# Kernel tuning notes

Hardware: AMD Instinct MI355X
Metric: run time of the kernel (lower is better)

The kernel has to match this reference:

```python
import jax, jax.numpy as jnp
import numpy as np

DELTA = 6.0      # 3 / (1 - alpha), alpha = 0.5
ETA = 1.0
MS_ITER = 3
D_FEAT = 256
N_PTS = 8192
X_SCALE = 0.06   # keeps ||x||^2 ~ 0.9 so exp(DELTA * X^T X) is well-conditioned


def setup_inputs() -> dict:
    key = jax.random.key(0)
    X = jax.random.normal(key, (D_FEAT, N_PTS), dtype=jnp.float32) * X_SCALE
    return {"X": X}


def _mean_shift_once(X):
    # X: [d, N]
    S = jnp.einsum('dn,dm->nm', X, X)          # X^T X, [N, N]
    K = jnp.exp(DELTA * S)                     # Gaussian-like affinity, [N, N]
    colsum = jnp.sum(K, axis=0)                # d = K^T @ ones  -> column sums, [N]
    # X @ P with P = (1-eta) I + eta K D_inv; D_inv = diag(1/colsum).
    # X @ K @ D_inv == (X @ K) / colsum (per-column scaling) -- no diag/eye materialized.
    XK = X @ K                                 # [d, N]
    return (1.0 - ETA) * X + ETA * (XK / colsum[None, :])


def reference(X):
    outs = []
    cur = X
    for _ in range(MS_ITER):
        cur = _mean_shift_once(cur)
        outs.append(cur)
    return tuple(outs)
```

## Files before the change

kernel.cpp:

```cpp
#include <hip/hip_runtime.h>
#include <hip/hip_bf16.h>
#include <stdint.h>

#define DFEAT 256
#define NPTS  8192

typedef __attribute__((ext_vector_type(8)))  short bf16x8;
typedef __attribute__((ext_vector_type(16))) float f32x16;
typedef __attribute__((ext_vector_type(4)))  int   int4v;
typedef __attribute__((ext_vector_type(4)))  float f32x4;

#define AS1 __attribute__((address_space(1)))
#define AS3 __attribute__((address_space(3)))

__device__ inline void dma16(const void* g, void* l) {
  __builtin_amdgcn_global_load_lds((const AS1 uint32_t*)g, (AS3 uint32_t*)l, 16, 0, 0);
}

__device__ inline uint16_t f2bf(float f) {
  union { float f; uint32_t u; } v; v.f = f;
  return (uint16_t)((v.u + 0x7FFFu + ((v.u >> 16) & 1u)) >> 16);
}

__device__ inline void barrier_lgkm_only() {
  __asm__ __volatile__("" ::: "memory");
  __builtin_amdgcn_s_waitcnt(0xC07F);
  __builtin_amdgcn_s_barrier();
  __asm__ __volatile__("" ::: "memory");
}


__global__ __launch_bounds__(512, 2) void ms_fused(
    const uint16_t* __restrict__ xaf,
    const uint16_t* __restrict__ xbf,
    float* __restrict__ num,
    float* __restrict__ cs)
{
  __shared__ __attribute__((aligned(16))) uint16_t XS[2][16384];
  __shared__ uint32_t Ps[128 * 33];

  const int tid  = threadIdx.x;
  const int w    = tid >> 6;
  const int lane = tid & 63;
  const int l31  = lane & 31;
  const int g    = lane >> 5;
  const int bid  = blockIdx.x;
  const int xcd  = bid & 7;
  const int q    = xcd >> 1;
  const int mt   = (bid >> 3) + ((xcd & 1) << 5);
  const int m0   = mt * 128;
  const int n_sub = w & 1;
  const int m_sub = w >> 1;

  const char* xafc = (const char*)xaf;
  const char* xbfc = (const char*)xbf;

  bf16x8 Bm[16];
  {
    const char* bp = xafc + (size_t)(m0 / 32 + m_sub) * 16384 + g * 512 + l31 * 16;
    #pragma unroll
    for (int ks = 0; ks < 16; ++ks)
      Bm[ks] = __builtin_bit_cast(bf16x8, *(const int4v*)(bp + ks * 1024));
  }

  f32x16 accO[4];
  #pragma unroll
  for (int m = 0; m < 4; ++m)
    #pragma unroll
    for (int r = 0; r < 16; ++r) accO[m][r] = 0.0f;
  float csacc = 0.0f;

  const int mrow = 32 * m_sub + l31;
  const int j0   = q * 32;

  {
    const char* src = xafc + (size_t)j0 * 32768;
    #pragma unroll
    for (int r = 0; r < 4; ++r)
      dma16(src + r * 8192 + tid * 16, (char*)XS[0] + r * 8192 + tid * 16);
  }

  for (int t = 0; t < 32; ++t) {
    const int jt  = j0 + t;
    const int cur = t & 1;
    __syncthreads();

    bf16x8 Xf[4];
    {
      const char* xp = xbfc + (size_t)w * 524288 + (size_t)(jt * 8 + g) * 512 + l31 * 16;
      #pragma unroll
      for (int ks = 0; ks < 4; ++ks)
        Xf[ks] = __builtin_bit_cast(bf16x8, *(const int4v*)(xp + ks * 1024));
    }
    __asm__ __volatile__("" ::: "memory");

    if (t < 31) {
      const char* src = xafc + (size_t)(jt + 1) * 32768;
      #pragma unroll
      for (int r = 0; r < 4; ++r)
        dma16(src + r * 8192 + tid * 16,
              (char*)XS[cur ^ 1] + r * 8192 + tid * 16);
    }

    f32x16 s0, s1;
    #pragma unroll
    for (int r = 0; r < 16; ++r) { s0[r] = 0.0f; s1[r] = 0.0f; }
    {
      const char* ap = (const char*)XS[cur] + n_sub * 16384 + g * 512 + l31 * 16;
      #pragma unroll
      for (int ks2 = 0; ks2 < 8; ++ks2) {
        bf16x8 A0 = __builtin_bit_cast(bf16x8, *(const int4v*)(ap + (2*ks2) * 1024));
        bf16x8 A1 = __builtin_bit_cast(bf16x8, *(const int4v*)(ap + (2*ks2+1) * 1024));
        s0 = __builtin_amdgcn_mfma_f32_32x32x16_bf16(A0, Bm[2*ks2],   s0, 0, 0, 0);
        s1 = __builtin_amdgcn_mfma_f32_32x32x16_bf16(A1, Bm[2*ks2+1], s1, 0, 0, 0);
      }
    }

    #pragma unroll
    for (int k = 0; k < 4; ++k) {
      float e0 = __expf(6.0f * (s0[4*k+0] + s1[4*k+0]));
      float e1 = __expf(6.0f * (s0[4*k+1] + s1[4*k+1]));
      float e2 = __expf(6.0f * (s0[4*k+2] + s1[4*k+2]));
      float e3 = __expf(6.0f * (s0[4*k+3] + s1[4*k+3]));
      csacc += (e0 + e1) + (e2 + e3);
      int base = mrow * 33 + 16 * n_sub + 4 * k + 2 * g;
      Ps[base]     = (uint32_t)f2bf(e0) | ((uint32_t)f2bf(e1) << 16);
      Ps[base + 1] = (uint32_t)f2bf(e2) | ((uint32_t)f2bf(e3) << 16);
    }
    barrier_lgkm_only();

    #pragma unroll
    for (int ks = 0; ks < 4; ++ks) {
      bf16x8 Bp[4];
      #pragma unroll
      for (int m = 0; m < 4; ++m) {
        int b = (32 * m + l31) * 33 + 8 * ks + 4 * g;
        union { uint32_t u[4]; bf16x8 v; } tb;
        tb.u[0] = Ps[b];     tb.u[1] = Ps[b + 1];
        tb.u[2] = Ps[b + 2]; tb.u[3] = Ps[b + 3];
        Bp[m] = tb.v;
      }
      #pragma unroll
      for (int m = 0; m < 4; ++m)
        accO[m] = __builtin_amdgcn_mfma_f32_32x32x16_bf16(Xf[ks], Bp[m], accO[m], 0,0,0);
    }
  }

  csacc += __shfl_xor(csacc, 32, 64);
  if (g == 0) atomicAdd(&cs[m0 + mrow], csacc);
  #pragma unroll
  for (int m = 0; m < 4; ++m)
    #pragma unroll
    for (int r = 0; r < 16; ++r) {
      int drow = 32 * w + (r & 3) + 8 * (r >> 2) + 4 * g;
      int mg   = m0 + 32 * m + l31;
      atomicAdd(&num[(size_t)drow * NPTS + mg], accO[m][r]);
    }
}

__global__ __launch_bounds__(256) void ms_combine(
    const float* __restrict__ src, const float* __restrict__ csr,
    float* __restrict__ csz, float* __restrict__ yout,
    float* __restrict__ numz,
    uint16_t* __restrict__ xaf, uint16_t* __restrict__ xbf,
    const int mode)
{
  __shared__ uint16_t T[64][66];
  const int tid = threadIdx.x;
  const int n0 = blockIdx.x * 64;
  const int d0 = blockIdx.y * 64;
  const bool divide = (mode >= 1);
  const bool emit   = (mode <= 1);

  #pragma unroll
  for (int i = 0; i < 4; ++i) {
    int e  = tid + i * 256;
    int dl = e >> 4, nq = e & 15;
    size_t idx = (size_t)(d0 + dl) * NPTS + (n0 + nq * 4);
    f32x4 v = *(const f32x4*)(src + idx);
    if (divide) {
      f32x4 c = *(const f32x4*)(csr + n0 + nq * 4);
      v /= c;
      *(f32x4*)(yout + idx) = v;
    }
    if (emit) {
      f32x4 z = {0.f, 0.f, 0.f, 0.f};
      *(f32x4*)(numz + idx) = z;
      #pragma unroll
      for (int k = 0; k < 4; ++k) T[dl][nq * 4 + k] = f2bf(v[k]);
    }
  }
  if (!emit) return;
  if (blockIdx.y == 0 && tid < 64) csz[n0 + tid] = 0.0f;
  __syncthreads();

  char* xafc = (char*)xaf;
  char* xbfc = (char*)xbf;
  #pragma unroll
  for (int i = 0; i < 2; ++i) {
    int c  = tid + i * 256;
    int nb = c >> 8, s2 = (c >> 5) & 7, ln = c & 31;
    union { uint32_t u[4]; int4v v; } pk;
    #pragma unroll
    for (int k = 0; k < 4; ++k) {
      uint32_t lo = T[s2 * 8 + 2 * k][nb * 32 + ln];
      uint32_t hi = T[s2 * 8 + 2 * k + 1][nb * 32 + ln];
      pk.u[k] = lo | (hi << 16);
    }
    *(int4v*)(xafc + (size_t)(n0 / 32 + nb) * 16384 +
              (size_t)(d0 / 8 + s2) * 512 + ln * 16) = pk.v;
  }
  #pragma unroll
  for (int i = 0; i < 2; ++i) {
    int c  = tid + i * 256;
    int db = c >> 8, uu = (c >> 5) & 7, ln = c & 31;
    const uint16_t* tr = &T[db * 32 + ln][uu * 8];
    union { uint32_t u[4]; int4v v; } pk;
    #pragma unroll
    for (int k = 0; k < 4; ++k)
      pk.u[k] = (uint32_t)tr[2 * k] | ((uint32_t)tr[2 * k + 1] << 16);
    *(int4v*)(xbfc + (size_t)(d0 / 32 + db) * 524288 +
              (size_t)(n0 / 8 + uu) * 512 + ln * 16) = pk.v;
  }
}

extern "C" void kernel_launch(void* const* d_in, const int* in_sizes, int n_in,
                              void* d_out, int out_size, void* d_ws, size_t ws_size,
                              hipStream_t stream)
{
  (void)in_sizes; (void)n_in; (void)out_size; (void)ws_size;
  const float* X = (const float*)d_in[0];
  float* out = (float*)d_out;
  char* ws = (char*)d_ws;
  uint16_t* xaf = (uint16_t*)(ws);
  uint16_t* xbf = (uint16_t*)(ws + (4u << 20));
  float*    num = (float*)   (ws + (8u << 20));
  float*    cs0 = (float*)   (ws + (16u << 20));
  float*    cs1 = (float*)   (ws + (16u << 20) + 32768);

  dim3 cgrid(NPTS / 64, DFEAT / 64);
  ms_combine<<<cgrid, 256, 0, stream>>>(X, nullptr, cs0, nullptr, num,
                                        xaf, xbf, 0);
  for (int it = 0; it < 3; ++it) {
    float* csA = (it & 1) ? cs1 : cs0;
    float* csB = (it & 1) ? cs0 : cs1;
    ms_fused<<<256, 512, 0, stream>>>(xaf, xbf, num, csA);
    ms_combine<<<cgrid, 256, 0, stream>>>(num, csA, csB,
                                          out + (size_t)it * DFEAT * NPTS,
                                          num, xaf, xbf, (it == 2) ? 2 : 1);
  }
}
```

Baseline: 367.9 us.

## Retile PV MFMA per wave, swizzle P in LDS, prescale X by sqrt6

Each wave now computes a 2x2 grid of 32x32 output tiles (two d-slices by two m-slices) instead of one d-slice across four m-slices, so each P fragment loaded from LDS feeds two MFMAs. The P buffer uses a 36-dword row stride with an XOR-style rotation, which allows 64-bit writes and 128-bit reads in place of scalar dword accesses. Bf16 packing now uses a single perm instruction with round-half-up instead of round-to-nearest-even. The factor 6 in the exponent is folded into the bf16 copy of X used for the Gram matrix by scaling it by sqrt(6), which changes rounding slightly and costs an extra LDS tile in the combine kernel.

```diff
diff --git a/kernel.cpp b/kernel.cpp
--- a/kernel.cpp
+++ b/kernel.cpp
@@ -20,6 +20,12 @@
 __device__ inline uint16_t f2bf(float f) {
   union { float f; uint32_t u; } v; v.f = f;
   return (uint16_t)((v.u + 0x7FFFu + ((v.u >> 16) & 1u)) >> 16);
+}
+
+__device__ inline uint32_t pack_bf2(float e0, float e1) {
+  uint32_t u0 = __builtin_bit_cast(uint32_t, e0) + 0x8000u;
+  uint32_t u1 = __builtin_bit_cast(uint32_t, e1) + 0x8000u;
+  return __builtin_amdgcn_perm(u1, u0, 0x07060302u);
 }
 
 __device__ inline void barrier_lgkm_only() {
@@ -37,7 +43,7 @@
     float* __restrict__ cs)
 {
   __shared__ __attribute__((aligned(16))) uint16_t XS[2][16384];
-  __shared__ uint32_t Ps[128 * 33];
+  __shared__ __attribute__((aligned(16))) uint32_t Ps[128 * 36];
 
   const int tid  = threadIdx.x;
   const int w    = tid >> 6;
@@ -51,6 +57,8 @@
   const int m0   = mt * 128;
   const int n_sub = w & 1;
   const int m_sub = w >> 1;
+  const int mh   = w & 1;
+  const int dq   = w >> 1;
 
   const char* xafc = (const char*)xaf;
   const char* xbfc = (const char*)xbf;
@@ -63,14 +71,17 @@
       Bm[ks] = __builtin_bit_cast(bf16x8, *(const int4v*)(bp + ks * 1024));
   }
 
-  f32x16 accO[4];
-  #pragma unroll
-  for (int m = 0; m < 4; ++m)
-    #pragma unroll
-    for (int r = 0; r < 16; ++r) accO[m][r] = 0.0f;
+  f32x16 accO[2][2];
+  #pragma unroll
+  for (int i = 0; i < 2; ++i)
+    #pragma unroll
+    for (int j = 0; j < 2; ++j)
+      #pragma unroll
+      for (int r = 0; r < 16; ++r) accO[i][j][r] = 0.0f;
   float csacc = 0.0f;
 
   const int mrow = 32 * m_sub + l31;
+  const int wr_rot = 4 * n_sub + (mrow >> 3);
   const int j0   = q * 32;
 
   {
@@ -85,12 +96,14 @@
     const int cur = t & 1;
     __syncthreads();
 
-    bf16x8 Xf[4];
-    {
-      const char* xp = xbfc + (size_t)w * 524288 + (size_t)(jt * 8 + g) * 512 + l31 * 16;
+    bf16x8 Xf[2][4];
+    #pragma unroll
+    for (int t2 = 0; t2 < 2; ++t2) {
+      const char* xp = xbfc + (size_t)(2 * dq + t2) * 524288 +
+                       (size_t)(jt * 8 + g) * 512 + l31 * 16;
       #pragma unroll
       for (int ks = 0; ks < 4; ++ks)
-        Xf[ks] = __builtin_bit_cast(bf16x8, *(const int4v*)(xp + ks * 1024));
+        Xf[t2][ks] = __builtin_bit_cast(bf16x8, *(const int4v*)(xp + ks * 1024));
     }
     __asm__ __volatile__("" ::: "memory");
 
@@ -118,44 +131,48 @@
 
     #pragma unroll
     for (int k = 0; k < 4; ++k) {
-      float e0 = __expf(6.0f * (s0[4*k+0] + s1[4*k+0]));
-      float e1 = __expf(6.0f * (s0[4*k+1] + s1[4*k+1]));
-      float e2 = __expf(6.0f * (s0[4*k+2] + s1[4*k+2]));
-      float e3 = __expf(6.0f * (s0[4*k+3] + s1[4*k+3]));
+      float e0 = __expf(s0[4*k+0] + s1[4*k+0]);
+      float e1 = __expf(s0[4*k+1] + s1[4*k+1]);
+      float e2 = __expf(s0[4*k+2] + s1[4*k+2]);
+      float e3 = __expf(s0[4*k+3] + s1[4*k+3]);
       csacc += (e0 + e1) + (e2 + e3);
-      int base = mrow * 33 + 16 * n_sub + 4 * k + 2 * g;
-      Ps[base]     = (uint32_t)f2bf(e0) | ((uint32_t)f2bf(e1) << 16);
-      Ps[base + 1] = (uint32_t)f2bf(e2) | ((uint32_t)f2bf(e3) << 16);
+      uint32_t lo = pack_bf2(e0, e1);
+      uint32_t hi = pack_bf2(e2, e3);
+      int dwi = mrow * 36 + (((wr_rot + k) & 7) << 2) + 2 * g;
+      *(uint64_t*)(&Ps[dwi]) = ((uint64_t)hi << 32) | lo;
     }
     barrier_lgkm_only();
 
     #pragma unroll
     for (int ks = 0; ks < 4; ++ks) {
-      bf16x8 Bp[4];
-      #pragma unroll
-      for (int m = 0; m < 4; ++m) {
-        int b = (32 * m + l31) * 33 + 8 * ks + 4 * g;
-        union { uint32_t u[4]; bf16x8 v; } tb;
-        tb.u[0] = Ps[b];     tb.u[1] = Ps[b + 1];
-        tb.u[2] = Ps[b + 2]; tb.u[3] = Ps[b + 3];
-        Bp[m] = tb.v;
-      }
-      #pragma unroll
-      for (int m = 0; m < 4; ++m)
-        accO[m] = __builtin_amdgcn_mfma_f32_32x32x16_bf16(Xf[ks], Bp[m], accO[m], 0,0,0);
+      bf16x8 Bp[2];
+      #pragma unroll
+      for (int mm = 0; mm < 2; ++mm) {
+        int m  = 32 * (2 * mh + mm) + l31;
+        int c  = 2 * ks + g;
+        int dwi = m * 36 + (((c + (m >> 3)) & 7) << 2);
+        Bp[mm] = __builtin_bit_cast(bf16x8, *(const int4v*)(&Ps[dwi]));
+      }
+      #pragma unroll
+      for (int t2 = 0; t2 < 2; ++t2) {
+        accO[t2][0] = __builtin_amdgcn_mfma_f32_32x32x16_bf16(Xf[t2][ks], Bp[0], accO[t2][0], 0,0,0);
+        accO[t2][1] = __builtin_amdgcn_mfma_f32_32x32x16_bf16(Xf[t2][ks], Bp[1], accO[t2][1], 0,0,0);
+      }
     }
   }
 
   csacc += __shfl_xor(csacc, 32, 64);
   if (g == 0) atomicAdd(&cs[m0 + mrow], csacc);
   #pragma unroll
-  for (int m = 0; m < 4; ++m)
-    #pragma unroll
-    for (int r = 0; r < 16; ++r) {
-      int drow = 32 * w + (r & 3) + 8 * (r >> 2) + 4 * g;
-      int mg   = m0 + 32 * m + l31;
-      atomicAdd(&num[(size_t)drow * NPTS + mg], accO[m][r]);
-    }
+  for (int t2 = 0; t2 < 2; ++t2)
+    #pragma unroll
+    for (int mm = 0; mm < 2; ++mm)
+      #pragma unroll
+      for (int r = 0; r < 16; ++r) {
+        int drow = 32 * (2 * dq + t2) + (r & 3) + 8 * (r >> 2) + 4 * g;
+        int mg   = m0 + 32 * (2 * mh + mm) + l31;
+        atomicAdd(&num[(size_t)drow * NPTS + mg], accO[t2][mm][r]);
+      }
 }
 
 __global__ __launch_bounds__(256) void ms_combine(
@@ -165,12 +182,14 @@
     uint16_t* __restrict__ xaf, uint16_t* __restrict__ xbf,
     const int mode)
 {
-  __shared__ uint16_t T[64][66];
+  __shared__ uint16_t T [64][66];
+  __shared__ uint16_t T6[64][66];
   const int tid = threadIdx.x;
   const int n0 = blockIdx.x * 64;
   const int d0 = blockIdx.y * 64;
   const bool divide = (mode >= 1);
   const bool emit   = (mode <= 1);
+  const float SQ6 = 2.4494897427831781f;
 
   #pragma unroll
   for (int i = 0; i < 4; ++i) {
@@ -187,7 +206,10 @@
       f32x4 z = {0.f, 0.f, 0.f, 0.f};
       *(f32x4*)(numz + idx) = z;
       #pragma unroll
-      for (int k = 0; k < 4; ++k) T[dl][nq * 4 + k] = f2bf(v[k]);
+      for (int k = 0; k < 4; ++k) {
+        T [dl][nq * 4 + k] = f2bf(v[k]);
+        T6[dl][nq * 4 + k] = f2bf(v[k] * SQ6);
+      }
     }
   }
   if (!emit) return;
@@ -203,8 +225,8 @@
     union { uint32_t u[4]; int4v v; } pk;
     #pragma unroll
     for (int k = 0; k < 4; ++k) {
-      uint32_t lo = T[s2 * 8 + 2 * k][nb * 32 + ln];
-      uint32_t hi = T[s2 * 8 + 2 * k + 1][nb * 32 + ln];
+      uint32_t lo = T6[s2 * 8 + 2 * k][nb * 32 + ln];
+      uint32_t hi = T6[s2 * 8 + 2 * k + 1][nb * 32 + ln];
       pk.u[k] = lo | (hi << 16);
     }
     *(int4v*)(xafc + (size_t)(n0 / 32 + nb) * 16384 +
```

Result: slower. 378.9 us (+3.0%).
